# Optimization experiments

Measured on AMD Instinct MI355X. Metric: run time of the kernel, lower is better.

## Reference

```python
import jax, jax.numpy as jnp
import numpy as np

D_MODEL = 1024
NUM_HEADS = 16
HEAD_DIM = D_MODEL // NUM_HEADS


def setup_inputs() -> dict:
    key = jax.random.key(0)
    k_x, k_wq, k_wo = jax.random.split(key, 3)
    x = jax.random.normal(k_x, (2, 2048, D_MODEL), dtype=jnp.float32)
    # Xavier-uniform init to mirror _reset_parameters
    lim_qkv = float(np.sqrt(6.0 / (D_MODEL + 3 * D_MODEL)))
    lim_o = float(np.sqrt(6.0 / (D_MODEL + D_MODEL)))
    w_qkv = jax.random.uniform(k_wq, (3 * D_MODEL, D_MODEL), jnp.float32, -lim_qkv, lim_qkv)
    b_qkv = jnp.zeros((3 * D_MODEL,), jnp.float32)
    w_o = jax.random.uniform(k_wo, (D_MODEL, D_MODEL), jnp.float32, -lim_o, lim_o)
    b_o = jnp.zeros((D_MODEL,), jnp.float32)
    return {"x": x, "w_qkv": w_qkv, "b_qkv": b_qkv, "w_o": w_o, "b_o": b_o}


def reference(x, w_qkv, b_qkv, w_o, b_o):
    B, T, C = x.shape
    H, Dh = NUM_HEADS, HEAD_DIM
    # Fused QKV projection: [B,T,3C]
    qkv = jnp.einsum('btc,oc->bto', x, w_qkv) + b_qkv
    qkv = qkv.reshape(B, T, 3, H, Dh)
    q = qkv[:, :, 0].transpose(0, 2, 1, 3)  # [B,H,T,Dh]
    k = qkv[:, :, 1].transpose(0, 2, 1, 3)
    v = qkv[:, :, 2].transpose(0, 2, 1, 3)
    scale = 1.0 / jnp.sqrt(jnp.asarray(Dh, x.dtype))
    scores = jnp.einsum('bhqd,bhkd->bhqk', q, k) * scale  # [B,H,T,T]
    attn = jax.nn.softmax(scores, axis=-1)
    out = jnp.einsum('bhqk,bhkd->bhqd', attn, v)  # [B,H,T,Dh]
    out = out.transpose(0, 2, 1, 3).reshape(B, T, C)
    return jnp.einsum('btc,oc->bto', out, w_o) + b_o
```

## Files before the change

kernel.cpp:

```cpp
#include <hip/hip_runtime.h>
#include <math.h>

#define SEQ   2048
#define BATCH 2
#define CDIM  1024
#define NH    16
#define DH    64
#define BH    (BATCH*NH)
#define KVB   64
#define QBLK  128

typedef __attribute__((ext_vector_type(8))) short bf16x8;
typedef __attribute__((ext_vector_type(4))) short s16x4;
typedef __attribute__((ext_vector_type(4))) float f32x4;

__device__ __forceinline__ short f2bf(float f) {
  union { float f; unsigned u; } v; v.f = f;
  unsigned r = (v.u + 0x7FFFu + ((v.u >> 16) & 1u)) >> 16;
  return (short)r;
}
__device__ __forceinline__ float bf2f(short s) {
  union { unsigned u; float f; } v; v.u = ((unsigned)(unsigned short)s) << 16;
  return v.f;
}
__device__ __forceinline__ void gload_lds16(const void* g, void* l) {
  __builtin_amdgcn_global_load_lds(
      (const __attribute__((address_space(1))) void*)g,
      (__attribute__((address_space(3))) void*)l, 16, 0, 0);
}

template<int R>
__device__ __forceinline__ void stage_tile(const short* __restrict__ g,
                                           short* __restrict__ lds, int tid) {
#pragma unroll
  for (int rd = 0; rd < R / 64; ++rd) {
    const int idx = rd * 256 + tid;
    const int row = idx >> 2, ch = idx & 3;
    const int sch = ch ^ ((row >> 1) & 3);
    gload_lds16(&g[(long)row * CDIM + sch * 8], &lds[idx * 8]);
  }
}
__device__ __forceinline__ bf16x8 frag(const short* __restrict__ lds,
                                       int row, int g) {
  const int sch = g ^ ((row >> 1) & 3);
  return *(const bf16x8*)&lds[row * 32 + sch * 8];
}

__device__ __forceinline__ int aswz(int row, int ch) {
  return (row << 6) + ((ch ^ (row & 7)) << 3);
}

__global__ __launch_bounds__(256)
void cvt_hilo(const float* __restrict__ in, short* __restrict__ hi,
              short* __restrict__ lo, int n4) {
  const int i = blockIdx.x * 256 + threadIdx.x;
  if (i >= n4) return;
  const float4 v = reinterpret_cast<const float4*>(in)[i];
  s16x4 h, l;
  h[0] = f2bf(v.x); h[1] = f2bf(v.y); h[2] = f2bf(v.z); h[3] = f2bf(v.w);
  l[0] = f2bf(v.x - bf2f(h[0]));
  l[1] = f2bf(v.y - bf2f(h[1]));
  l[2] = f2bf(v.z - bf2f(h[2]));
  l[3] = f2bf(v.w - bf2f(h[3]));
  reinterpret_cast<s16x4*>(hi)[i] = h;
  reinterpret_cast<s16x4*>(lo)[i] = l;
}

__global__ __launch_bounds__(256)
void qkv_mfma(const short* __restrict__ xh, const short* __restrict__ xl,
              const short* __restrict__ wh, const short* __restrict__ wl,
              const float* __restrict__ bias,
              short* __restrict__ qh, short* __restrict__ ql,
              short* __restrict__ kh, short* __restrict__ kl,
              short* __restrict__ vt) {
  __shared__ short S[2][4][128 * 32];
  const int tid  = threadIdx.x;
  const int wave = tid >> 6, lane = tid & 63;
  const int l15  = lane & 15, g = lane >> 4;
  const int wr   = wave >> 1, wc = wave & 1;
  const int m0   = blockIdx.y * 128, n0 = blockIdx.x * 128;

  const short* Abh = xh + (long)m0 * CDIM;
  const short* Abl = xl + (long)m0 * CDIM;
  const short* Bbh = wh + (long)n0 * CDIM;
  const short* Bbl = wl + (long)n0 * CDIM;

  f32x4 acc[4][4];
#pragma unroll
  for (int mi = 0; mi < 4; ++mi)
#pragma unroll
    for (int ni = 0; ni < 4; ++ni) {
      acc[mi][ni][0] = 0.f; acc[mi][ni][1] = 0.f;
      acc[mi][ni][2] = 0.f; acc[mi][ni][3] = 0.f;
    }

  stage_tile<128>(Abh, S[0][0], tid);
  stage_tile<128>(Abl, S[0][1], tid);
  stage_tile<128>(Bbh, S[0][2], tid);
  stage_tile<128>(Bbl, S[0][3], tid);
  __syncthreads();

  for (int k = 0; k < CDIM / 32; ++k) {
    const int cur = k & 1;
    if (k < CDIM / 32 - 1) {
      const int k1 = (k + 1) * 32;
      stage_tile<128>(Abh + k1, S[cur ^ 1][0], tid);
      stage_tile<128>(Abl + k1, S[cur ^ 1][1], tid);
      stage_tile<128>(Bbh + k1, S[cur ^ 1][2], tid);
      stage_tile<128>(Bbl + k1, S[cur ^ 1][3], tid);
    }
    bf16x8 ah[4], al2[4], bh2[4], bl2[4];
#pragma unroll
    for (int mi = 0; mi < 4; ++mi) {
      const int r = wr * 64 + mi * 16 + l15;
      ah[mi]  = frag(S[cur][0], r, g);
      al2[mi] = frag(S[cur][1], r, g);
    }
#pragma unroll
    for (int ni = 0; ni < 4; ++ni) {
      const int r = wc * 64 + ni * 16 + l15;
      bh2[ni] = frag(S[cur][2], r, g);
      bl2[ni] = frag(S[cur][3], r, g);
    }
#pragma unroll
    for (int mi = 0; mi < 4; ++mi)
#pragma unroll
      for (int ni = 0; ni < 4; ++ni) {
        acc[mi][ni] = __builtin_amdgcn_mfma_f32_16x16x32_bf16(
            ah[mi], bh2[ni], acc[mi][ni], 0, 0, 0);
        acc[mi][ni] = __builtin_amdgcn_mfma_f32_16x16x32_bf16(
            al2[mi], bh2[ni], acc[mi][ni], 0, 0, 0);
        acc[mi][ni] = __builtin_amdgcn_mfma_f32_16x16x32_bf16(
            ah[mi], bl2[ni], acc[mi][ni], 0, 0, 0);
      }
    __syncthreads();
  }

  const int s = n0 >> 10;
  const int hbase = (n0 & 1023) >> 6;
  if (s < 2) {
    short* hb = (s == 0) ? qh : kh;
    short* lb = (s == 0) ? ql : kl;
    const float sc = (s == 0) ? 0.125f : 1.0f;
    float bv[4];
#pragma unroll
    for (int ni = 0; ni < 4; ++ni) bv[ni] = bias[n0 + wc * 64 + ni * 16 + l15];
    short* T = &S[0][0][0];
#pragma unroll
    for (int p = 0; p < 2; ++p) {
#pragma unroll
      for (int mi = 0; mi < 4; ++mi)
#pragma unroll
        for (int ni = 0; ni < 4; ++ni)
#pragma unroll
          for (int r = 0; r < 4; ++r) {
            const int row = wr * 64 + mi * 16 + g * 4 + r;
            const int col = wc * 64 + ni * 16 + l15;
            const float v = (acc[mi][ni][r] + bv[ni]) * sc;
            const short hv = f2bf(v);
            T[row * 136 + col] = (p == 0) ? hv : f2bf(v - bf2f(hv));
          }
      __syncthreads();
      short* dst = (p == 0) ? hb : lb;
#pragma unroll
      for (int it = 0; it < 8; ++it) {
        const int idx = it * 256 + tid;
        const int row = idx >> 4, c16 = idx & 15;
        const bf16x8 vv = *(const bf16x8*)&T[row * 136 + c16 * 8];
        const int h = hbase + (c16 >> 3), dh0 = (c16 & 7) * 8;
        const int t = m0 + row, bi = t >> 11, tt = t & 2047;
        *(bf16x8*)&dst[(((long)(bi * NH + h)) * SEQ + tt) * DH + dh0] = vv;
      }
      __syncthreads();
    }
  } else {
#pragma unroll
    for (int ni = 0; ni < 4; ++ni) {
      const int n_g = n0 + wc * 64 + ni * 16 + l15;
      const int o = n_g & 1023, h = o >> 6, dh = o & 63;
      const float bvv = bias[n_g];
#pragma unroll
      for (int mi = 0; mi < 4; ++mi) {
        const int mr = m0 + wr * 64 + mi * 16 + g * 4;
        const int bi = mr >> 11, t = mr & 2047;
        s16x4 pv;
#pragma unroll
        for (int r = 0; r < 4; ++r) pv[r] = f2bf(acc[mi][ni][r] + bvv);
        *(s16x4*)&vt[(((long)(bi * NH + h)) * DH + dh) * SEQ + t] = pv;
      }
    }
  }
}

__global__ __launch_bounds__(512)
void fattn_mfma(const short* __restrict__ qhg, const short* __restrict__ qlg,
                const short* __restrict__ khg, const short* __restrict__ klg,
                const short* __restrict__ vtg,
                short* __restrict__ abh, short* __restrict__ abl) {
  __shared__ short Khs[KVB * 64];
  __shared__ short Kls[KVB * 64];
  __shared__ short Vts[DH * 64];
  __shared__ short Ps[QBLK * 64];

  const int tid  = threadIdx.x;
  const int wave = tid >> 6;
  const int lane = tid & 63;
  const int l15  = lane & 15;
  const int g    = lane >> 4;
  const int bh   = blockIdx.x;
  const int q0   = blockIdx.y * QBLK;
  const int qw   = q0 + wave * 16;

  const long qrow = ((long)bh * SEQ + qw + l15) * DH;
  bf16x8 Qh[2], Ql[2];
#pragma unroll
  for (int c = 0; c < 2; ++c) {
    Qh[c] = *(const bf16x8*)&qhg[qrow + c * 32 + g * 8];
    Ql[c] = *(const bf16x8*)&qlg[qrow + c * 32 + g * 8];
  }

  f32x4 o[4];
#pragma unroll
  for (int d = 0; d < 4; ++d) { o[d][0] = 0.f; o[d][1] = 0.f; o[d][2] = 0.f; o[d][3] = 0.f; }
  float mrun[4], lrun[4];
#pragma unroll
  for (int r = 0; r < 4; ++r) { mrun[r] = -1e30f; lrun[r] = 0.f; }

  const int srow = tid >> 3;
  const int sch  = tid & 7;
  const int wdst = aswz(srow, sch);
  const long kgbase = (long)bh * SEQ * DH + (long)srow * DH + sch * 8;
  const long vgbase = ((long)bh * DH + srow) * SEQ + sch * 8;

  bf16x8 rk = *(const bf16x8*)&khg[kgbase];
  bf16x8 rl = *(const bf16x8*)&klg[kgbase];
  bf16x8 rv = *(const bf16x8*)&vtg[vgbase];

  for (int kt = 0; kt < SEQ / KVB; ++kt) {
    if (kt) __syncthreads();
    *(bf16x8*)&Khs[wdst] = rk;
    *(bf16x8*)&Kls[wdst] = rl;
    *(bf16x8*)&Vts[wdst] = rv;
    if (kt + 1 < SEQ / KVB) {
      const long ko = kgbase + (long)(kt + 1) * KVB * DH;
      rk = *(const bf16x8*)&khg[ko];
      rl = *(const bf16x8*)&klg[ko];
      rv = *(const bf16x8*)&vtg[vgbase + (kt + 1) * KVB];
    }
    __syncthreads();

    f32x4 s[4];
    __builtin_amdgcn_s_setprio(1);
#pragma unroll
    for (int kc = 0; kc < 4; ++kc) {
      f32x4 a; a[0] = 0.f; a[1] = 0.f; a[2] = 0.f; a[3] = 0.f;
#pragma unroll
      for (int c = 0; c < 2; ++c) {
        const int adr = aswz(kc * 16 + l15, c * 4 + g);
        bf16x8 kb = *(const bf16x8*)&Khs[adr];
        bf16x8 lb = *(const bf16x8*)&Kls[adr];
        a = __builtin_amdgcn_mfma_f32_16x16x32_bf16(Qh[c], kb, a, 0, 0, 0);
        a = __builtin_amdgcn_mfma_f32_16x16x32_bf16(Ql[c], kb, a, 0, 0, 0);
        a = __builtin_amdgcn_mfma_f32_16x16x32_bf16(Qh[c], lb, a, 0, 0, 0);
      }
      s[kc] = a;
    }
    __builtin_amdgcn_s_setprio(0);

#pragma unroll
    for (int r = 0; r < 4; ++r) {
      float mt = fmaxf(fmaxf(s[0][r], s[1][r]), fmaxf(s[2][r], s[3][r]));
#pragma unroll
      for (int msk = 1; msk <= 8; msk <<= 1)
        mt = fmaxf(mt, __shfl_xor(mt, msk));
      const float mn = fmaxf(mrun[r], mt);
      const float al = __expf(mrun[r] - mn);
      float p0 = __expf(s[0][r] - mn);
      float p1 = __expf(s[1][r] - mn);
      float p2 = __expf(s[2][r] - mn);
      float p3 = __expf(s[3][r] - mn);
      lrun[r] = lrun[r] * al + ((p0 + p1) + (p2 + p3));
      mrun[r] = mn;
#pragma unroll
      for (int d = 0; d < 4; ++d) o[d][r] *= al;
      const int prow = wave * 16 + g * 4 + r;
      const int rx = prow & 7;
      const int pbase = (prow << 6) + (l15 & 7);
      const int hi8 = l15 >> 3;
      Ps[pbase + (((0 + hi8) ^ rx) << 3)] = f2bf(p0);
      Ps[pbase + (((2 + hi8) ^ rx) << 3)] = f2bf(p1);
      Ps[pbase + (((4 + hi8) ^ rx) << 3)] = f2bf(p2);
      Ps[pbase + (((6 + hi8) ^ rx) << 3)] = f2bf(p3);
    }

    __builtin_amdgcn_s_setprio(1);
#pragma unroll
    for (int kk = 0; kk < 2; ++kk) {
      bf16x8 pf = *(const bf16x8*)&Ps[aswz(wave * 16 + l15, kk * 4 + g)];
#pragma unroll
      for (int d = 0; d < 4; ++d) {
        bf16x8 vf = *(const bf16x8*)&Vts[aswz(d * 16 + l15, kk * 4 + g)];
        o[d] = __builtin_amdgcn_mfma_f32_16x16x32_bf16(pf, vf, o[d], 0, 0, 0);
      }
    }
    __builtin_amdgcn_s_setprio(0);
  }

  const int b = bh >> 4, hh = bh & 15;
#pragma unroll
  for (int r = 0; r < 4; ++r) {
    float rs = lrun[r];
#pragma unroll
    for (int msk = 1; msk <= 8; msk <<= 1)
      rs += __shfl_xor(rs, msk);
    const float inv = 1.0f / rs;
    const int t = qw + g * 4 + r;
    const long base = ((long)(b * SEQ + t)) * CDIM + hh * DH + l15;
#pragma unroll
    for (int d = 0; d < 4; ++d) {
      const float v = o[d][r] * inv;
      const short hv = f2bf(v);
      abh[base + d * 16] = hv;
      abl[base + d * 16] = f2bf(v - bf2f(hv));
    }
  }
}

__global__ __launch_bounds__(256)
void out_mfma(const short* __restrict__ ah, const short* __restrict__ al,
              const short* __restrict__ wh, const short* __restrict__ wl,
              const float* __restrict__ bias, float* __restrict__ out) {
  __shared__ short S[2][12288];
  const int tid  = threadIdx.x;
  const int wave = tid >> 6, lane = tid & 63;
  const int l15  = lane & 15, g = lane >> 4;
  const int wr   = wave >> 1, wc = wave & 1;
  const int m0   = blockIdx.y * 128, n0 = blockIdx.x * 64;

  const short* Abh = ah + (long)m0 * CDIM;
  const short* Abl = al + (long)m0 * CDIM;
  const short* Bbh = wh + (long)n0 * CDIM;
  const short* Bbl = wl + (long)n0 * CDIM;

  f32x4 acc[4][2];
#pragma unroll
  for (int mi = 0; mi < 4; ++mi)
#pragma unroll
    for (int ni = 0; ni < 2; ++ni) {
      acc[mi][ni][0] = 0.f; acc[mi][ni][1] = 0.f;
      acc[mi][ni][2] = 0.f; acc[mi][ni][3] = 0.f;
    }

  stage_tile<128>(Abh, &S[0][0], tid);
  stage_tile<128>(Abl, &S[0][4096], tid);
  stage_tile<64>(Bbh, &S[0][8192], tid);
  stage_tile<64>(Bbl, &S[0][10240], tid);
  __syncthreads();

  for (int k = 0; k < CDIM / 32; ++k) {
    const int cur = k & 1;
    if (k < CDIM / 32 - 1) {
      const int k1 = (k + 1) * 32;
      stage_tile<128>(Abh + k1, &S[cur ^ 1][0], tid);
      stage_tile<128>(Abl + k1, &S[cur ^ 1][4096], tid);
      stage_tile<64>(Bbh + k1, &S[cur ^ 1][8192], tid);
      stage_tile<64>(Bbl + k1, &S[cur ^ 1][10240], tid);
    }
    bf16x8 af[4], af2[4], bf1[2], bf2[2];
#pragma unroll
    for (int mi = 0; mi < 4; ++mi) {
      const int r = wr * 64 + mi * 16 + l15;
      af[mi]  = frag(&S[cur][0], r, g);
      af2[mi] = frag(&S[cur][4096], r, g);
    }
#pragma unroll
    for (int ni = 0; ni < 2; ++ni) {
      const int r = wc * 32 + ni * 16 + l15;
      bf1[ni] = frag(&S[cur][8192], r, g);
      bf2[ni] = frag(&S[cur][10240], r, g);
    }
#pragma unroll
    for (int mi = 0; mi < 4; ++mi)
#pragma unroll
      for (int ni = 0; ni < 2; ++ni) {
        acc[mi][ni] = __builtin_amdgcn_mfma_f32_16x16x32_bf16(
            af[mi], bf1[ni], acc[mi][ni], 0, 0, 0);
        acc[mi][ni] = __builtin_amdgcn_mfma_f32_16x16x32_bf16(
            af2[mi], bf1[ni], acc[mi][ni], 0, 0, 0);
        acc[mi][ni] = __builtin_amdgcn_mfma_f32_16x16x32_bf16(
            af[mi], bf2[ni], acc[mi][ni], 0, 0, 0);
      }
    __syncthreads();
  }

#pragma unroll
  for (int ni = 0; ni < 2; ++ni) {
    const int n = n0 + wc * 32 + ni * 16 + l15;
    const float bv = bias[n];
#pragma unroll
    for (int mi = 0; mi < 4; ++mi) {
#pragma unroll
      for (int r = 0; r < 4; ++r) {
        const int m = m0 + wr * 64 + mi * 16 + g * 4 + r;
        out[(long)m * CDIM + n] = acc[mi][ni][r] + bv;
      }
    }
  }
}

__global__ __launch_bounds__(256)
void qkv_gemm_f32(const float* __restrict__ x, const float* __restrict__ w,
                  const float* __restrict__ bias,
                  short* __restrict__ qh, short* __restrict__ ql,
                  short* __restrict__ kh, short* __restrict__ kl,
                  short* __restrict__ vt) {
  __shared__ float As[16][65];
  __shared__ float Bs[16][65];
  const int tid = threadIdx.x;
  const int tx = tid & 15, ty = tid >> 4;
  const int m0 = blockIdx.y * 64;
  const int n0 = blockIdx.x * 64;
  const int lr = tid >> 2;
  const int lc = (tid & 3) << 2;
  float acc[4][4] = {};
  const float* ap = x + (long)(m0 + lr) * CDIM + lc;
  const float* bp = w + (long)(n0 + lr) * CDIM + lc;
  for (int k0 = 0; k0 < CDIM; k0 += 16) {
    float4 av = *reinterpret_cast<const float4*>(ap + k0);
    float4 bv = *reinterpret_cast<const float4*>(bp + k0);
    __syncthreads();
    As[lc + 0][lr] = av.x; As[lc + 1][lr] = av.y;
    As[lc + 2][lr] = av.z; As[lc + 3][lr] = av.w;
    Bs[lc + 0][lr] = bv.x; Bs[lc + 1][lr] = bv.y;
    Bs[lc + 2][lr] = bv.z; Bs[lc + 3][lr] = bv.w;
    __syncthreads();
#pragma unroll
    for (int kk = 0; kk < 16; ++kk) {
      float a[4], bb[4];
#pragma unroll
      for (int i = 0; i < 4; ++i) a[i] = As[kk][ty * 4 + i];
#pragma unroll
      for (int j = 0; j < 4; ++j) bb[j] = Bs[kk][tx * 4 + j];
#pragma unroll
      for (int i = 0; i < 4; ++i)
#pragma unroll
        for (int j = 0; j < 4; ++j)
          acc[i][j] = fmaf(a[i], bb[j], acc[i][j]);
    }
  }
  const int s = n0 >> 10;
  const int hh = (n0 & 1023) >> 6;
  const float4 bq = *reinterpret_cast<const float4*>(&bias[n0 + tx * 4]);
  if (s < 2) {
    const float scale = (s == 0) ? 0.125f : 1.0f;
    short* hb = (s == 0) ? qh : kh;
    short* lb = (s == 0) ? ql : kl;
#pragma unroll
    for (int i = 0; i < 4; ++i) {
      const int m = m0 + ty * 4 + i;
      const int bi = m >> 11, t = m & 2047;
      float v0 = (acc[i][0] + bq.x) * scale;
      float v1 = (acc[i][1] + bq.y) * scale;
      float v2 = (acc[i][2] + bq.z) * scale;
      float v3 = (acc[i][3] + bq.w) * scale;
      s16x4 hv, lv;
      hv[0] = f2bf(v0); hv[1] = f2bf(v1); hv[2] = f2bf(v2); hv[3] = f2bf(v3);
      lv[0] = f2bf(v0 - bf2f(hv[0]));
      lv[1] = f2bf(v1 - bf2f(hv[1]));
      lv[2] = f2bf(v2 - bf2f(hv[2]));
      lv[3] = f2bf(v3 - bf2f(hv[3]));
      const long base = (((long)(bi * NH + hh)) * SEQ + t) * DH + tx * 4;
      *(s16x4*)&hb[base] = hv;
      *(s16x4*)&lb[base] = lv;
    }
  } else {
#pragma unroll
    for (int i = 0; i < 4; ++i) {
      const int m = m0 + ty * 4 + i;
      const int bi = m >> 11, t = m & 2047;
      float vv[4] = {acc[i][0] + bq.x, acc[i][1] + bq.y,
                     acc[i][2] + bq.z, acc[i][3] + bq.w};
#pragma unroll
      for (int j = 0; j < 4; ++j)
        vt[((long)(bi * NH + hh) * DH + tx * 4 + j) * SEQ + t] = f2bf(vv[j]);
    }
  }
}

__global__ __launch_bounds__(256)
void out_gemm_f32(const short* __restrict__ ah, const short* __restrict__ al,
                  const float* __restrict__ w,
                  const float* __restrict__ bias, float* __restrict__ out) {
  __shared__ float As[16][65];
  __shared__ float Bs[16][65];
  const int tid = threadIdx.x;
  const int tx = tid & 15, ty = tid >> 4;
  const int m0 = blockIdx.y * 64;
  const int n0 = blockIdx.x * 64;
  const int lr = tid >> 2;
  const int lc = (tid & 3) << 2;
  float acc[4][4] = {};
  const long arow = (long)(m0 + lr) * CDIM + lc;
  const float* bp = w + (long)(n0 + lr) * CDIM + lc;
  for (int k0 = 0; k0 < CDIM; k0 += 16) {
    s16x4 hv = *(const s16x4*)&ah[arow + k0];
    s16x4 lv = *(const s16x4*)&al[arow + k0];
    float4 bv = *reinterpret_cast<const float4*>(bp + k0);
    __syncthreads();
#pragma unroll
    for (int j = 0; j < 4; ++j) As[lc + j][lr] = bf2f(hv[j]) + bf2f(lv[j]);
    Bs[lc + 0][lr] = bv.x; Bs[lc + 1][lr] = bv.y;
    Bs[lc + 2][lr] = bv.z; Bs[lc + 3][lr] = bv.w;
    __syncthreads();
#pragma unroll
    for (int kk = 0; kk < 16; ++kk) {
      float av2[4], bb[4];
#pragma unroll
      for (int i = 0; i < 4; ++i) av2[i] = As[kk][ty * 4 + i];
#pragma unroll
      for (int j = 0; j < 4; ++j) bb[j] = Bs[kk][tx * 4 + j];
#pragma unroll
      for (int i = 0; i < 4; ++i)
#pragma unroll
        for (int j = 0; j < 4; ++j)
          acc[i][j] = fmaf(av2[i], bb[j], acc[i][j]);
    }
  }
  const float4 bq = *reinterpret_cast<const float4*>(&bias[n0 + tx * 4]);
#pragma unroll
  for (int i = 0; i < 4; ++i) {
    const int m = m0 + ty * 4 + i;
    float4 v;
    v.x = acc[i][0] + bq.x; v.y = acc[i][1] + bq.y;
    v.z = acc[i][2] + bq.z; v.w = acc[i][3] + bq.w;
    *reinterpret_cast<float4*>(&out[(long)m * CDIM + n0 + tx * 4]) = v;
  }
}

extern "C" void kernel_launch(void* const* d_in, const int* in_sizes, int n_in,
                              void* d_out, int out_size, void* d_ws, size_t ws_size,
                              hipStream_t stream) {
  (void)in_sizes; (void)n_in; (void)out_size;
  const float* x     = (const float*)d_in[0];
  const float* w_qkv = (const float*)d_in[1];
  const float* b_qkv = (const float*)d_in[2];
  const float* w_o   = (const float*)d_in[3];
  const float* b_o   = (const float*)d_in[4];
  float* out = (float*)d_out;

  const size_t NEED = 71303168;
  if (ws_size >= NEED) {
    short* base = (short*)d_ws;
    short* xh  = base;
    short* xl  = base + 4194304;
    short* wqh = base + 8388608;
    short* wql = base + 11534336;
    short* qh  = base + 14680064;
    short* ql  = base + 18874368;
    short* kh  = base + 23068672;
    short* kl  = base + 27262976;
    short* vt  = base + 31457280;
    short* woh = wqh;
    short* wol = wqh + 1048576;
    short* abh = xh;
    short* abl = xl;

    cvt_hilo<<<4096, 256, 0, stream>>>(x, xh, xl, 1048576);
    cvt_hilo<<<3072, 256, 0, stream>>>(w_qkv, wqh, wql, 786432);
    qkv_mfma<<<dim3(24, 32), 256, 0, stream>>>(xh, xl, wqh, wql, b_qkv,
                                               qh, ql, kh, kl, vt);
    cvt_hilo<<<1024, 256, 0, stream>>>(w_o, woh, wol, 262144);
    fattn_mfma<<<dim3(BH, SEQ / QBLK), 512, 0, stream>>>(qh, ql, kh, kl, vt,
                                                         abh, abl);
    out_mfma<<<dim3(16, 32), 256, 0, stream>>>(abh, abl, woh, wol, b_o, out);
  } else {
    short* qh  = (short*)d_ws;
    short* ql  = qh + 4194304;
    short* kh  = ql + 4194304;
    short* kl  = kh + 4194304;
    short* vt  = kl + 4194304;
    short* abh = vt + 4194304;
    short* abl = abh + 4194304;

    qkv_gemm_f32<<<dim3(48, 64), 256, 0, stream>>>(x, w_qkv, b_qkv,
                                                   qh, ql, kh, kl, vt);
    fattn_mfma<<<dim3(BH, SEQ / QBLK), 512, 0, stream>>>(qh, ql, kh, kl, vt,
                                                         abh, abl);
    out_gemm_f32<<<dim3(16, 64), 256, 0, stream>>>(abh, abl, w_o, b_o, out);
  }
}
```

Before: 246.2 us.

## Double-buffer K/V via direct global-to-LDS loads and use exp2 softmax

The flash-attention loop now double-buffers K/V tiles in LDS and fills them with global_load_lds, so the next tile is fetched directly into LDS while the current one is computed. This removes the register staging and one barrier per iteration. Q is pre-scaled by log2(e)/sqrt(Dh) so the softmax can use the raw v_exp_f32 (exp2). The running-max rescale is skipped when no row max grows in the wave, and P is converted with a packed bf16 instruction. LDS use roughly doubles for K/V, and the skipped rescale and exp2 path change numerics slightly.

Result: no change. 242.5 us (-1.5%).

```diff
diff --git a/kernel.cpp b/kernel.cpp
--- a/kernel.cpp
+++ b/kernel.cpp
@@ -10,6 +10,8 @@
 #define KVB   64
 #define QBLK  128
 
+#define QSCALE 0.18033688011112042f
+
 typedef __attribute__((ext_vector_type(8))) short bf16x8;
 typedef __attribute__((ext_vector_type(4))) short s16x4;
 typedef __attribute__((ext_vector_type(4))) float f32x4;
@@ -22,6 +24,13 @@
 __device__ __forceinline__ float bf2f(short s) {
   union { unsigned u; float f; } v; v.u = ((unsigned)(unsigned short)s) << 16;
   return v.f;
+}
+__device__ __forceinline__ float fexp2(float x) {
+  float r; asm("v_exp_f32 %0, %1" : "=v"(r) : "v"(x)); return r;
+}
+__device__ __forceinline__ unsigned cvtpk_bf16(float a, float b) {
+  unsigned r; asm("v_cvt_pk_bf16_f32 %0, %1, %2" : "=v"(r) : "v"(a), "v"(b));
+  return r;
 }
 __device__ __forceinline__ void gload_lds16(const void* g, void* l) {
   __builtin_amdgcn_global_load_lds(
@@ -141,7 +150,7 @@
   if (s < 2) {
     short* hb = (s == 0) ? qh : kh;
     short* lb = (s == 0) ? ql : kl;
-    const float sc = (s == 0) ? 0.125f : 1.0f;
+    const float sc = (s == 0) ? QSCALE : 1.0f;
     float bv[4];
 #pragma unroll
     for (int ni = 0; ni < 4; ++ni) bv[ni] = bias[n0 + wc * 64 + ni * 16 + l15];
@@ -197,9 +206,9 @@
                 const short* __restrict__ khg, const short* __restrict__ klg,
                 const short* __restrict__ vtg,
                 short* __restrict__ abh, short* __restrict__ abl) {
-  __shared__ short Khs[KVB * 64];
-  __shared__ short Kls[KVB * 64];
-  __shared__ short Vts[DH * 64];
+  __shared__ short Khs[2][KVB * 64];
+  __shared__ short Kls[2][KVB * 64];
+  __shared__ short Vts[2][DH * 64];
   __shared__ short Ps[QBLK * 64];
 
   const int tid  = threadIdx.x;
@@ -227,28 +236,27 @@
   for (int r = 0; r < 4; ++r) { mrun[r] = -1e30f; lrun[r] = 0.f; }
 
   const int srow = tid >> 3;
-  const int sch  = tid & 7;
-  const int wdst = aswz(srow, sch);
-  const long kgbase = (long)bh * SEQ * DH + (long)srow * DH + sch * 8;
-  const long vgbase = ((long)bh * DH + srow) * SEQ + sch * 8;
-
-  bf16x8 rk = *(const bf16x8*)&khg[kgbase];
-  bf16x8 rl = *(const bf16x8*)&klg[kgbase];
-  bf16x8 rv = *(const bf16x8*)&vtg[vgbase];
-
+  const int gch  = (tid & 7) ^ (srow & 7);
+  const long ksrc0 = (long)bh * SEQ * DH + (long)srow * DH + gch * 8;
+  const long vsrc0 = ((long)bh * DH + srow) * SEQ + gch * 8;
+  const int  ldst  = tid * 8;
+
+  gload_lds16(&khg[ksrc0], &Khs[0][ldst]);
+  gload_lds16(&klg[ksrc0], &Kls[0][ldst]);
+  gload_lds16(&vtg[vsrc0], &Vts[0][ldst]);
+  __syncthreads();
+
+  int cur = 0;
   for (int kt = 0; kt < SEQ / KVB; ++kt) {
-    if (kt) __syncthreads();
-    *(bf16x8*)&Khs[wdst] = rk;
-    *(bf16x8*)&Kls[wdst] = rl;
-    *(bf16x8*)&Vts[wdst] = rv;
     if (kt + 1 < SEQ / KVB) {
-      const long ko = kgbase + (long)(kt + 1) * KVB * DH;
-      rk = *(const bf16x8*)&khg[ko];
-      rl = *(const bf16x8*)&klg[ko];
-      rv = *(const bf16x8*)&vtg[vgbase + (kt + 1) * KVB];
-    }
-    __syncthreads();
-
+      const long ko = ksrc0 + (long)(kt + 1) * (KVB * DH);
+      gload_lds16(&khg[ko], &Khs[cur ^ 1][ldst]);
+      gload_lds16(&klg[ko], &Kls[cur ^ 1][ldst]);
+      gload_lds16(&vtg[vsrc0 + (kt + 1) * KVB], &Vts[cur ^ 1][ldst]);
+    }
+
+    const short* Kc = Khs[cur];
+    const short* Lc = Kls[cur];
     f32x4 s[4];
     __builtin_amdgcn_s_setprio(1);
 #pragma unroll
@@ -257,8 +265,8 @@
 #pragma unroll
       for (int c = 0; c < 2; ++c) {
         const int adr = aswz(kc * 16 + l15, c * 4 + g);
-        bf16x8 kb = *(const bf16x8*)&Khs[adr];
-        bf16x8 lb = *(const bf16x8*)&Kls[adr];
+        bf16x8 kb = *(const bf16x8*)&Kc[adr];
+        bf16x8 lb = *(const bf16x8*)&Lc[adr];
         a = __builtin_amdgcn_mfma_f32_16x16x32_bf16(Qh[c], kb, a, 0, 0, 0);
         a = __builtin_amdgcn_mfma_f32_16x16x32_bf16(Ql[c], kb, a, 0, 0, 0);
         a = __builtin_amdgcn_mfma_f32_16x16x32_bf16(Qh[c], lb, a, 0, 0, 0);
@@ -267,43 +275,62 @@
     }
     __builtin_amdgcn_s_setprio(0);
 
+    float mt[4];
 #pragma unroll
     for (int r = 0; r < 4; ++r) {
-      float mt = fmaxf(fmaxf(s[0][r], s[1][r]), fmaxf(s[2][r], s[3][r]));
+      float m_ = fmaxf(fmaxf(s[0][r], s[1][r]), fmaxf(s[2][r], s[3][r]));
 #pragma unroll
       for (int msk = 1; msk <= 8; msk <<= 1)
-        mt = fmaxf(mt, __shfl_xor(mt, msk));
-      const float mn = fmaxf(mrun[r], mt);
-      const float al = __expf(mrun[r] - mn);
-      float p0 = __expf(s[0][r] - mn);
-      float p1 = __expf(s[1][r] - mn);
-      float p2 = __expf(s[2][r] - mn);
-      float p3 = __expf(s[3][r] - mn);
-      lrun[r] = lrun[r] * al + ((p0 + p1) + (p2 + p3));
-      mrun[r] = mn;
-#pragma unroll
-      for (int d = 0; d < 4; ++d) o[d][r] *= al;
+        m_ = fmaxf(m_, __shfl_xor(m_, msk));
+      mt[r] = m_;
+    }
+    const bool grow = (mt[0] > mrun[0]) | (mt[1] > mrun[1]) |
+                      (mt[2] > mrun[2]) | (mt[3] > mrun[3]);
+    if (__any(grow)) {
+#pragma unroll
+      for (int r = 0; r < 4; ++r) {
+        const float mn = fmaxf(mrun[r], mt[r]);
+        const float al = fexp2(mrun[r] - mn);
+        lrun[r] *= al;
+        mrun[r] = mn;
+#pragma unroll
+        for (int d = 0; d < 4; ++d) o[d][r] *= al;
+      }
+    }
+#pragma unroll
+    for (int r = 0; r < 4; ++r) {
+      const float p0 = fexp2(s[0][r] - mrun[r]);
+      const float p1 = fexp2(s[1][r] - mrun[r]);
+      const float p2 = fexp2(s[2][r] - mrun[r]);
+      const float p3 = fexp2(s[3][r] - mrun[r]);
+      lrun[r] += (p0 + p1) + (p2 + p3);
+      const unsigned w01 = cvtpk_bf16(p0, p1);
+      const unsigned w23 = cvtpk_bf16(p2, p3);
       const int prow = wave * 16 + g * 4 + r;
       const int rx = prow & 7;
       const int pbase = (prow << 6) + (l15 & 7);
       const int hi8 = l15 >> 3;
-      Ps[pbase + (((0 + hi8) ^ rx) << 3)] = f2bf(p0);
-      Ps[pbase + (((2 + hi8) ^ rx) << 3)] = f2bf(p1);
-      Ps[pbase + (((4 + hi8) ^ rx) << 3)] = f2bf(p2);
-      Ps[pbase + (((6 + hi8) ^ rx) << 3)] = f2bf(p3);
-    }
-
+      Ps[pbase + (((0 + hi8) ^ rx) << 3)] = (short)w01;
+      Ps[pbase + (((2 + hi8) ^ rx) << 3)] = (short)(w01 >> 16);
+      Ps[pbase + (((4 + hi8) ^ rx) << 3)] = (short)w23;
+      Ps[pbase + (((6 + hi8) ^ rx) << 3)] = (short)(w23 >> 16);
+    }
+
+    const short* Vc = Vts[cur];
     __builtin_amdgcn_s_setprio(1);
 #pragma unroll
     for (int kk = 0; kk < 2; ++kk) {
       bf16x8 pf = *(const bf16x8*)&Ps[aswz(wave * 16 + l15, kk * 4 + g)];
 #pragma unroll
       for (int d = 0; d < 4; ++d) {
-        bf16x8 vf = *(const bf16x8*)&Vts[aswz(d * 16 + l15, kk * 4 + g)];
+        bf16x8 vf = *(const bf16x8*)&Vc[aswz(d * 16 + l15, kk * 4 + g)];
         o[d] = __builtin_amdgcn_mfma_f32_16x16x32_bf16(pf, vf, o[d], 0, 0, 0);
       }
     }
     __builtin_amdgcn_s_setprio(0);
+
+    __syncthreads();
+    cur ^= 1;
   }
 
   const int b = bh >> 4, hh = bh & 15;
@@ -452,7 +479,7 @@
   const int hh = (n0 & 1023) >> 6;
   const float4 bq = *reinterpret_cast<const float4*>(&bias[n0 + tx * 4]);
   if (s < 2) {
-    const float scale = (s == 0) ? 0.125f : 1.0f;
+    const float scale = (s == 0) ? QSCALE : 1.0f;
     short* hb = (s == 0) ? qh : kh;
     short* lb = (s == 0) ? ql : kl;
 #pragma unroll
```
